# Optimization experiments

Measured on AMD Instinct MI355X. Metric: run time of the kernel, lower is better.

## Reference

```python
import jax, jax.numpy as jnp
import numpy as np

EMBED = 1024
HEADS = 16
HEAD_DIM = EMBED // HEADS


def setup_inputs() -> dict:
    key = jax.random.key(0)
    ks = jax.random.split(key, 12)
    B, S = 2, 2048
    s = 1.0 / np.sqrt(EMBED)
    inp = {
        "query": jax.random.normal(ks[0], (B, S, EMBED), jnp.float32),
        "key_": jax.random.normal(ks[1], (B, S, EMBED), jnp.float32),
        "value": jax.random.normal(ks[2], (B, S, EMBED), jnp.float32),
        "Wq": jax.random.normal(ks[3], (EMBED, EMBED), jnp.float32) * s,
        "bq": jnp.zeros((EMBED,), jnp.float32),
        "Wk": jax.random.normal(ks[4], (EMBED, EMBED), jnp.float32) * s,
        "bk": jnp.zeros((EMBED,), jnp.float32),
        "Wv": jax.random.normal(ks[5], (EMBED, EMBED), jnp.float32) * s,
        "bv": jnp.zeros((EMBED,), jnp.float32),
        "head_mixing": jnp.ones((HEADS, HEADS), jnp.float32) / HEADS,
        "Wo": jax.random.normal(ks[6], (EMBED, EMBED), jnp.float32) * s,
        "bo": jnp.zeros((EMBED,), jnp.float32),
    }
    return inp


def reference(query, key_, value, Wq, bq, Wk, bk, Wv, bv, head_mixing, Wo, bo):
    B, Sq, _ = query.shape
    Sk = key_.shape[1]
    # projections -> [B, H, S, D]
    q = (query @ Wq + bq).reshape(B, Sq, HEADS, HEAD_DIM).transpose(0, 2, 1, 3)
    k = (key_ @ Wk + bk).reshape(B, Sk, HEADS, HEAD_DIM).transpose(0, 2, 1, 3)
    v = (value @ Wv + bv).reshape(B, Sk, HEADS, HEAD_DIM).transpose(0, 2, 1, 3)
    scores = jnp.einsum("bhqd,bhkd->bhqk", q, k) / jnp.sqrt(jnp.float32(HEAD_DIM))
    attn = jax.nn.softmax(scores, axis=-1)  # [B,H,Sq,Sk]; dropout is identity (eval)
    mix = jax.nn.softmax(head_mixing, axis=-1)  # [G,H], softmax over source heads
    mixed = jnp.einsum("bhqk,gh->bgqk", attn, mix)
    ctx = jnp.einsum("bgqk,bgkd->bgqd", mixed, v)  # [B,H,Sq,D]
    ctx = ctx.transpose(0, 2, 1, 3).reshape(B, Sq, EMBED)
    return ctx @ Wo + bo
```

## Files before the change

kernel.cpp:

```cpp
#include <hip/hip_runtime.h>
#include <hip/hip_bf16.h>
#include <cstdint>
#include <cstddef>


typedef __bf16 bf16_t;
typedef __bf16 bf16x8 __attribute__((ext_vector_type(8)));
typedef float f32x4 __attribute__((ext_vector_type(4)));

#define B_ 2
#define S_ 2048
#define E_ 1024
#define H_ 16
#define D_ 64
#define HSTR 18
#define GSTR 580

static __device__ __forceinline__ f32x4 mfma16(bf16x8 a, bf16x8 b, f32x4 c) {
  return __builtin_amdgcn_mfma_f32_16x16x32_bf16(a, b, c, 0, 0, 0);
}

static __device__ __forceinline__ void gload_lds16(const void* g, void* l) {
  __builtin_amdgcn_global_load_lds(
      (const __attribute__((address_space(1))) void*)g,
      (__attribute__((address_space(3))) void*)l, 16, 0, 0);
}

__global__ void mix_kernel(const float* __restrict__ hm, float* __restrict__ mixw) {
  int g = threadIdx.x;
  if (g < H_) {
    float v[H_]; float mx = -1e30f;
    for (int h = 0; h < H_; h++) { v[h] = hm[g * H_ + h]; mx = fmaxf(mx, v[h]); }
    float s = 0.f;
    for (int h = 0; h < H_; h++) { v[h] = __expf(v[h] - mx); s += v[h]; }
    float inv = 1.f / s;
    for (int h = 0; h < H_; h++) mixw[g * H_ + h] = v[h] * inv;
  }
}

__global__ void convw_kernel(const float* __restrict__ w0, const float* __restrict__ w1,
                             const float* __restrict__ w2, const float* __restrict__ w3,
                             bf16_t* __restrict__ t0, bf16_t* __restrict__ t1,
                             bf16_t* __restrict__ t2, bf16_t* __restrict__ t3) {
  __shared__ float t[32][33];
  const int tx = threadIdx.x & 31, ty = threadIdx.x >> 5;
  const int z = blockIdx.z;
  const float* W  = (z == 0) ? w0 : (z == 1) ? w1 : (z == 2) ? w2 : w3;
  bf16_t*      Wt = (z == 0) ? t0 : (z == 1) ? t1 : (z == 2) ? t2 : t3;
  const int k0 = blockIdx.x * 32, n0 = blockIdx.y * 32;
#pragma unroll
  for (int i = 0; i < 4; i++)
    t[ty + i * 8][tx] = W[(size_t)(k0 + ty + i * 8) * E_ + n0 + tx];
  __syncthreads();
#pragma unroll
  for (int i = 0; i < 4; i++)
    Wt[(size_t)(n0 + ty + i * 8) * E_ + k0 + tx] = (bf16_t)t[tx][ty + i * 8];
}

__global__ void convin_kernel(const float* __restrict__ q, const float* __restrict__ k,
                              const float* __restrict__ v,
                              bf16_t* __restrict__ qo, bf16_t* __restrict__ ko,
                              bf16_t* __restrict__ vo) {
  const int z = blockIdx.y;
  const float* src = (z == 0) ? q : (z == 1) ? k : v;
  bf16_t*      dst = (z == 0) ? qo : (z == 1) ? ko : vo;
  const size_t i = ((size_t)blockIdx.x * 256 + threadIdx.x) * 8;
  f32x4 a = *(const f32x4*)&src[i];
  f32x4 b = *(const f32x4*)&src[i + 4];
  bf16x8 o;
#pragma unroll
  for (int j = 0; j < 4; j++) { o[j] = (bf16_t)a[j]; o[4 + j] = (bf16_t)b[j]; }
  *(bf16x8*)&dst[i] = o;
}

__global__ void transpose_v_kernel(const bf16_t* __restrict__ Vp, bf16_t* __restrict__ Vt) {
  __shared__ bf16_t t[32][33];
  const int tx = threadIdx.x & 31, ty = threadIdx.x >> 5;
  const int z = blockIdx.z, b = z >> 4, g = z & 15;
  const int s0 = blockIdx.x * 32, d0 = blockIdx.y * 32;
  const bf16_t* src = Vp + (size_t)b * S_ * E_ + g * 64;
  bf16_t* dst = Vt + (size_t)z * 64 * S_;
#pragma unroll
  for (int i = 0; i < 4; i++)
    t[ty + i * 8][tx] = src[(size_t)(s0 + ty + i * 8) * E_ + d0 + tx];
  __syncthreads();
#pragma unroll
  for (int i = 0; i < 4; i++)
    dst[(size_t)(d0 + ty + i * 8) * S_ + s0 + tx] = t[tx][ty + i * 8];
}

struct GemmSec {
  const void* A; const void* A2; const float* bias; const bf16_t* W; void* C; float scale;
};

template <bool AF32, bool OF32, bool ASUM>
__global__ __launch_bounds__(256) void gemm_kernel(GemmSec s0, GemmSec s1, GemmSec s2) {
  const int z = blockIdx.z;
  GemmSec p = (z == 0) ? s0 : ((z == 1) ? s1 : s2);
  const int tid = threadIdx.x;
  const int wave = tid >> 6, lane = tid & 63;
  const int ln = lane & 15, qd = lane >> 4;
  const int wm = wave >> 1, wn = wave & 1;
  const int row0 = blockIdx.y * 128, col0 = blockIdx.x * 128;

  __shared__ __align__(16) bf16_t As[128 * 32];
  __shared__ __align__(16) bf16_t Bs[128 * 32];

  f32x4 z4 = {0.f, 0.f, 0.f, 0.f};
  f32x4 acc[4][4];
#pragma unroll
  for (int i = 0; i < 4; i++)
#pragma unroll
    for (int j = 0; j < 4; j++) acc[i][j] = z4;

  for (int ks = 0; ks < E_ / 32; ks++) {
    const int kk = ks * 32;
#pragma unroll
    for (int cc = 0; cc < 2; cc++) {
      const int c = tid + cc * 256;
      const int r = c >> 2, kc = (c & 3) * 8;
      if (AF32) {
        const float* Af = (const float*)p.A;
        f32x4 f0 = *(const f32x4*)&Af[(size_t)(row0 + r) * E_ + kk + kc];
        f32x4 f1 = *(const f32x4*)&Af[(size_t)(row0 + r) * E_ + kk + kc + 4];
        if (ASUM) {
          const float* Ag = (const float*)p.A2;
          f0 += *(const f32x4*)&Ag[(size_t)(row0 + r) * E_ + kk + kc];
          f1 += *(const f32x4*)&Ag[(size_t)(row0 + r) * E_ + kk + kc + 4];
        }
        bf16x8 v;
#pragma unroll
        for (int j = 0; j < 4; j++) { v[j] = (bf16_t)f0[j]; v[4 + j] = (bf16_t)f1[j]; }
        *(bf16x8*)&As[r * 32 + kc] = v;
      } else {
        const bf16_t* Ab = (const bf16_t*)p.A;
        gload_lds16(&Ab[(size_t)(row0 + r) * E_ + kk + kc], &As[r * 32 + kc]);
      }
    }
#pragma unroll
    for (int cc = 0; cc < 2; cc++) {
      const int c = tid + cc * 256;
      const int r = c >> 2, kc = (c & 3) * 8;
      gload_lds16(&p.W[(size_t)(col0 + r) * E_ + kk + kc], &Bs[r * 32 + kc]);
    }
    __syncthreads();
    bf16x8 af[4], bfr[4];
#pragma unroll
    for (int mt = 0; mt < 4; mt++) af[mt] = *(const bf16x8*)&As[(wm * 64 + mt * 16 + ln) * 32 + qd * 8];
#pragma unroll
    for (int nt = 0; nt < 4; nt++) bfr[nt] = *(const bf16x8*)&Bs[(wn * 64 + nt * 16 + ln) * 32 + qd * 8];
#pragma unroll
    for (int mt = 0; mt < 4; mt++)
#pragma unroll
      for (int nt = 0; nt < 4; nt++)
        acc[mt][nt] = mfma16(af[mt], bfr[nt], acc[mt][nt]);
    __syncthreads();
  }
#pragma unroll
  for (int nt = 0; nt < 4; nt++) {
    int col = col0 + wn * 64 + nt * 16 + ln;
    float bias_v = p.bias[col];
#pragma unroll
    for (int mt = 0; mt < 4; mt++) {
      int row = row0 + wm * 64 + mt * 16 + qd * 4;
#pragma unroll
      for (int r = 0; r < 4; r++) {
        float v = (acc[mt][nt][r] + bias_v) * p.scale;
        if (OF32) ((float*)p.C)[(size_t)(row + r) * E_ + col] = v;
        else      ((bf16_t*)p.C)[(size_t)(row + r) * E_ + col] = (bf16_t)v;
      }
    }
  }
}

__global__ __launch_bounds__(256, 4) void pass1_kernel(const bf16_t* __restrict__ Qp,
                                                       const bf16_t* __restrict__ Kp,
                                                       float* __restrict__ Z) {
  const int qc = blockIdx.x;
  const int bh = blockIdx.y;
  const int b = bh >> 4, h = bh & 15;
  const int tid = threadIdx.x;
  const int wave = tid >> 6, lane = tid & 63;
  const int ln = lane & 15, qd = lane >> 4;
  const size_t rowbase = (size_t)b * S_;
  const int qbase = qc * 64 + wave * 16;

  bf16x8 qf[2];
#pragma unroll
  for (int db = 0; db < 2; db++)
    qf[db] = *(const bf16x8*)&Qp[(rowbase + qbase + ln) * E_ + h * 64 + db * 32 + qd * 8];

  float l[4] = {0.f, 0.f, 0.f, 0.f};

  for (int kt = 0; kt < S_ / 64; kt++) {
    bf16x8 kf[4][2];
#pragma unroll
    for (int nt = 0; nt < 4; nt++)
#pragma unroll
      for (int db = 0; db < 2; db++)
        kf[nt][db] = *(const bf16x8*)&Kp[(rowbase + kt * 64 + nt * 16 + ln) * E_ + h * 64 + db * 32 + qd * 8];
    f32x4 sc[4];
#pragma unroll
    for (int nt = 0; nt < 4; nt++) {
      f32x4 c0 = {0.f, 0.f, 0.f, 0.f};
      c0 = mfma16(qf[0], kf[nt][0], c0);
      sc[nt] = mfma16(qf[1], kf[nt][1], c0);
    }
#pragma unroll
    for (int r = 0; r < 4; r++)
      l[r] += __expf(sc[0][r]) + __expf(sc[1][r]) + __expf(sc[2][r]) + __expf(sc[3][r]);
  }
#pragma unroll
  for (int r = 0; r < 4; r++) {
    float ll = l[r];
    for (int mask = 1; mask < 16; mask <<= 1) ll += __shfl_xor(ll, mask);
    if (ln == 0) {
      int q = qbase + qd * 4 + r;
      Z[(size_t)bh * S_ + q] = __logf(ll);
    }
  }
}

__global__ __launch_bounds__(512) void pass2_kernel(const bf16_t* __restrict__ Qp,
                                                    const bf16_t* __restrict__ Kp,
                                                    const bf16_t* __restrict__ Vt,
                                                    const float* __restrict__ Z,
                                                    const float* __restrict__ mixw,
                                                    float* __restrict__ pp) {
  const int id = blockIdx.x;
  const int kg = id & 1;
  const int qt = (id >> 1) & 127;
  const int b  = id >> 8;
  const int q0 = qt * 16;

  const int tid = threadIdx.x;
  const int wave = tid >> 6, lane = tid & 63;
  const int ln = lane & 15, qd = lane >> 4;
  const int h0 = wave * 2;

  __shared__ __align__(16) bf16_t Pt[16 * 32 * HSTR];
  __shared__ __align__(16) bf16_t Mx[16 * GSTR];

  const size_t rowbase = (size_t)b * S_;
  const int kbase = kg * (S_ / 2);

  bf16x8 mixA;
#pragma unroll
  for (int j = 0; j < 8; j++) mixA[j] = (bf16_t)0.f;
  if (qd < 2) {
#pragma unroll
    for (int j = 0; j < 8; j++) mixA[j] = (bf16_t)mixw[ln * 16 + qd * 8 + j];
  }

  bf16x8 qf[2][2];
#pragma unroll
  for (int hh = 0; hh < 2; hh++)
#pragma unroll
    for (int db = 0; db < 2; db++)
      qf[hh][db] = *(const bf16x8*)&Qp[(rowbase + q0 + ln) * E_ + (h0 + hh) * 64 + db * 32 + qd * 8];

  float Zr[2][4];
#pragma unroll
  for (int hh = 0; hh < 2; hh++)
#pragma unroll
    for (int r = 0; r < 4; r++)
      Zr[hh][r] = Z[((size_t)(b * H_ + h0 + hh)) * S_ + q0 + qd * 4 + r];

  f32x4 z4 = {0.f, 0.f, 0.f, 0.f};
  f32x4 cacc[2][4];
#pragma unroll
  for (int gg = 0; gg < 2; gg++)
#pragma unroll
    for (int nt = 0; nt < 4; nt++) cacc[gg][nt] = z4;

  const int hsw = (h0 ^ ((qd & 1) << 3));

  for (int t = 0; t < S_ / 64; t++) {
    const int kb = kbase + t * 32;
    uint32_t pk[2][4];
#pragma unroll
    for (int hh = 0; hh < 2; hh++) {
      bf16x8 kf[2][2];
#pragma unroll
      for (int n2 = 0; n2 < 2; n2++)
#pragma unroll
        for (int db = 0; db < 2; db++)
          kf[n2][db] = *(const bf16x8*)&Kp[(rowbase + kb + n2 * 16 + ln) * E_ + (h0 + hh) * 64 + db * 32 + qd * 8];
#pragma unroll
      for (int n2 = 0; n2 < 2; n2++) {
        f32x4 c0;
        c0[0] = -Zr[hh][0]; c0[1] = -Zr[hh][1]; c0[2] = -Zr[hh][2]; c0[3] = -Zr[hh][3];
        c0 = mfma16(qf[hh][0], kf[n2][0], c0);
        c0 = mfma16(qf[hh][1], kf[n2][1], c0);
#pragma unroll
        for (int r = 0; r < 4; r++) {
          uint32_t e = (uint32_t)__builtin_bit_cast(unsigned short, (bf16_t)__expf(c0[r]));
          if (hh == 0) pk[n2][r] = e;
          else         pk[n2][r] |= (e << 16);
        }
      }
    }
#pragma unroll
    for (int n2 = 0; n2 < 2; n2++)
#pragma unroll
      for (int r = 0; r < 4; r++) {
        const int col = (qd * 4 + r) * 32 + n2 * 16 + ln;
        *(uint32_t*)&Pt[col * HSTR + hsw] = pk[n2][r];
      }
    __syncthreads();
    f32x4 mm[4];
#pragma unroll
    for (int i = 0; i < 4; i++) {
      const int cc = wave * 4 + i;
      const int q  = cc >> 1;
      const int k  = (cc & 1) * 16 + ln;
      bf16x8 pb;
      if (qd < 2) {
        const int hblk = (qd * 8) ^ (((q >> 2) & 1) << 3);
        pb = *(const bf16x8*)&Pt[(q * 32 + k) * HSTR + hblk];
      } else {
#pragma unroll
        for (int j = 0; j < 8; j++) pb[j] = (bf16_t)0.f;
      }
      mm[i] = mfma16(mixA, pb, z4);
    }
#pragma unroll
    for (int i = 0; i < 4; i++) {
      const int cc = wave * 4 + i;
      const int q  = cc >> 1;
      const int k  = (cc & 1) * 16 + ln;
#pragma unroll
      for (int r = 0; r < 4; r++)
        Mx[(qd * 4 + r) * GSTR + q * 36 + k] = (bf16_t)mm[i][r];
    }
    __syncthreads();
#pragma unroll
    for (int gg = 0; gg < 2; gg++) {
      bf16x8 af = *(const bf16x8*)&Mx[(h0 + gg) * GSTR + ln * 36 + qd * 8];
#pragma unroll
      for (int nt = 0; nt < 4; nt++) {
        bf16x8 vf = *(const bf16x8*)&Vt[((size_t)((b * H_ + h0 + gg) * 64 + nt * 16 + ln)) * S_ + kb + qd * 8];
        cacc[gg][nt] = mfma16(af, vf, cacc[gg][nt]);
      }
    }
  }
  float* dst = pp + (size_t)kg * B_ * S_ * E_;
#pragma unroll
  for (int gg = 0; gg < 2; gg++)
#pragma unroll
    for (int nt = 0; nt < 4; nt++)
#pragma unroll
      for (int r = 0; r < 4; r++)
        dst[(rowbase + q0 + qd * 4 + r) * E_ + (h0 + gg) * 64 + nt * 16 + ln] = cacc[gg][nt][r];
}

extern "C" void kernel_launch(void* const* d_in, const int* in_sizes, int n_in,
                              void* d_out, int out_size, void* d_ws, size_t ws_size,
                              hipStream_t stream) {
  const float* query = (const float*)d_in[0];
  const float* key_  = (const float*)d_in[1];
  const float* value = (const float*)d_in[2];
  const float* Wq = (const float*)d_in[3];
  const float* bq = (const float*)d_in[4];
  const float* Wk = (const float*)d_in[5];
  const float* bk = (const float*)d_in[6];
  const float* Wv = (const float*)d_in[7];
  const float* bv = (const float*)d_in[8];
  const float* hm = (const float*)d_in[9];
  const float* Wo = (const float*)d_in[10];
  const float* bo = (const float*)d_in[11];
  float* out = (float*)d_out;

  char* ws = (char*)d_ws;
  size_t off = 0;
  auto alloc = [&](size_t bytes) -> void* {
    void* p = ws + off;
    off += (bytes + 255) & ~(size_t)255;
    return p;
  };
  float*  MIXW = (float*) alloc(256 * 4);
  float*  Zb   = (float*) alloc((size_t)B_ * H_ * S_ * 4);
  bf16_t* Qp   = (bf16_t*)alloc((size_t)B_ * S_ * E_ * 2);
  bf16_t* Kp   = (bf16_t*)alloc((size_t)B_ * S_ * E_ * 2);
  bf16_t* Vtt  = (bf16_t*)alloc((size_t)B_ * S_ * E_ * 2);
  bf16_t* Wqt  = (bf16_t*)alloc((size_t)E_ * E_ * 2);
  bf16_t* Wkt  = (bf16_t*)alloc((size_t)E_ * E_ * 2);
  bf16_t* Wvt  = (bf16_t*)alloc((size_t)E_ * E_ * 2);
  bf16_t* Wot  = (bf16_t*)alloc((size_t)E_ * E_ * 2);
  float*  PP   = (float*) alloc((size_t)2 * B_ * S_ * E_ * 4);
  const size_t NELEM = (size_t)B_ * S_ * E_;
  bf16_t* Vp = (bf16_t*)PP;
  bf16_t* Qb = Vp + NELEM;
  bf16_t* Kb = Vp + 2 * NELEM;
  bf16_t* Vb = Vp + 3 * NELEM;
  (void)in_sizes; (void)n_in; (void)out_size; (void)ws_size;

  mix_kernel<<<1, 256, 0, stream>>>(hm, MIXW);
  convw_kernel<<<dim3(32, 32, 4), 256, 0, stream>>>(Wq, Wk, Wv, Wo, Wqt, Wkt, Wvt, Wot);
  convin_kernel<<<dim3(2048, 3), 256, 0, stream>>>(query, key_, value, Qb, Kb, Vb);

  GemmSec sq{Qb, nullptr, bq, Wqt, Qp, 0.125f};
  GemmSec sk{Kb, nullptr, bk, Wkt, Kp, 1.f};
  GemmSec sv{Vb, nullptr, bv, Wvt, Vp, 1.f};
  gemm_kernel<false, false, false><<<dim3(8, 32, 3), 256, 0, stream>>>(sq, sk, sv);

  transpose_v_kernel<<<dim3(64, 2, 32), 256, 0, stream>>>(Vp, Vtt);
  pass1_kernel<<<dim3(32, 32, 1), 256, 0, stream>>>(Qp, Kp, Zb);
  pass2_kernel<<<dim3(512, 1, 1), 512, 0, stream>>>(Qp, Kp, Vtt, Zb, MIXW, PP);

  float* PP1 = PP + (size_t)B_ * S_ * E_;
  GemmSec so{PP, PP1, bo, Wot, out, 1.f};
  gemm_kernel<true, true, true><<<dim3(8, 32, 1), 256, 0, stream>>>(so, so, so);
}
```

Measured before the change: 569.7 us.

## Fuse prep kernels and write transposed V directly from projection GEMM epilogue

Merges the head-mixing softmax, weight transpose/convert and input conversion into one prep kernel, which cuts two launches. It also removes the separate V transpose kernel: the V projection GEMM epilogue writes bf16x4 chunks straight into the per-head transposed layout. This avoids a full read and write of the V projection plus one launch. The trade-off is that the transposed stores are strided across S and may coalesce less well than the original row-major stores.

```diff
diff --git a/kernel.cpp b/kernel.cpp
--- a/kernel.cpp
+++ b/kernel.cpp
@@ -6,6 +6,7 @@
 
 typedef __bf16 bf16_t;
 typedef __bf16 bf16x8 __attribute__((ext_vector_type(8)));
+typedef __bf16 bf16x4 __attribute__((ext_vector_type(4)));
 typedef float f32x4 __attribute__((ext_vector_type(4)));
 
 #define B_ 2
@@ -26,74 +27,64 @@
       (__attribute__((address_space(3))) void*)l, 16, 0, 0);
 }
 
-__global__ void mix_kernel(const float* __restrict__ hm, float* __restrict__ mixw) {
-  int g = threadIdx.x;
-  if (g < H_) {
-    float v[H_]; float mx = -1e30f;
-    for (int h = 0; h < H_; h++) { v[h] = hm[g * H_ + h]; mx = fmaxf(mx, v[h]); }
-    float s = 0.f;
-    for (int h = 0; h < H_; h++) { v[h] = __expf(v[h] - mx); s += v[h]; }
-    float inv = 1.f / s;
-    for (int h = 0; h < H_; h++) mixw[g * H_ + h] = v[h] * inv;
-  }
-}
-
-__global__ void convw_kernel(const float* __restrict__ w0, const float* __restrict__ w1,
-                             const float* __restrict__ w2, const float* __restrict__ w3,
-                             bf16_t* __restrict__ t0, bf16_t* __restrict__ t1,
-                             bf16_t* __restrict__ t2, bf16_t* __restrict__ t3) {
+__global__ void prep_kernel(const float* __restrict__ hm, float* __restrict__ mixw,
+                            const float* __restrict__ w0, const float* __restrict__ w1,
+                            const float* __restrict__ w2, const float* __restrict__ w3,
+                            bf16_t* __restrict__ t0, bf16_t* __restrict__ t1,
+                            bf16_t* __restrict__ t2, bf16_t* __restrict__ t3,
+                            const float* __restrict__ q, const float* __restrict__ k,
+                            const float* __restrict__ v,
+                            bf16_t* __restrict__ qo, bf16_t* __restrict__ ko,
+                            bf16_t* __restrict__ vo) {
   __shared__ float t[32][33];
-  const int tx = threadIdx.x & 31, ty = threadIdx.x >> 5;
+  const int tid = threadIdx.x;
   const int z = blockIdx.z;
-  const float* W  = (z == 0) ? w0 : (z == 1) ? w1 : (z == 2) ? w2 : w3;
-  bf16_t*      Wt = (z == 0) ? t0 : (z == 1) ? t1 : (z == 2) ? t2 : t3;
-  const int k0 = blockIdx.x * 32, n0 = blockIdx.y * 32;
-#pragma unroll
-  for (int i = 0; i < 4; i++)
-    t[ty + i * 8][tx] = W[(size_t)(k0 + ty + i * 8) * E_ + n0 + tx];
-  __syncthreads();
-#pragma unroll
-  for (int i = 0; i < 4; i++)
-    Wt[(size_t)(n0 + ty + i * 8) * E_ + k0 + tx] = (bf16_t)t[tx][ty + i * 8];
-}
-
-__global__ void convin_kernel(const float* __restrict__ q, const float* __restrict__ k,
-                              const float* __restrict__ v,
-                              bf16_t* __restrict__ qo, bf16_t* __restrict__ ko,
-                              bf16_t* __restrict__ vo) {
-  const int z = blockIdx.y;
-  const float* src = (z == 0) ? q : (z == 1) ? k : v;
-  bf16_t*      dst = (z == 0) ? qo : (z == 1) ? ko : vo;
-  const size_t i = ((size_t)blockIdx.x * 256 + threadIdx.x) * 8;
-  f32x4 a = *(const f32x4*)&src[i];
-  f32x4 b = *(const f32x4*)&src[i + 4];
-  bf16x8 o;
-#pragma unroll
-  for (int j = 0; j < 4; j++) { o[j] = (bf16_t)a[j]; o[4 + j] = (bf16_t)b[j]; }
-  *(bf16x8*)&dst[i] = o;
-}
-
-__global__ void transpose_v_kernel(const bf16_t* __restrict__ Vp, bf16_t* __restrict__ Vt) {
-  __shared__ bf16_t t[32][33];
-  const int tx = threadIdx.x & 31, ty = threadIdx.x >> 5;
-  const int z = blockIdx.z, b = z >> 4, g = z & 15;
-  const int s0 = blockIdx.x * 32, d0 = blockIdx.y * 32;
-  const bf16_t* src = Vp + (size_t)b * S_ * E_ + g * 64;
-  bf16_t* dst = Vt + (size_t)z * 64 * S_;
-#pragma unroll
-  for (int i = 0; i < 4; i++)
-    t[ty + i * 8][tx] = src[(size_t)(s0 + ty + i * 8) * E_ + d0 + tx];
-  __syncthreads();
-#pragma unroll
-  for (int i = 0; i < 4; i++)
-    dst[(size_t)(d0 + ty + i * 8) * S_ + s0 + tx] = t[tx][ty + i * 8];
+  if (z < 4) {
+    const int tx = tid & 31, ty = tid >> 5;
+    const float* W  = (z == 0) ? w0 : (z == 1) ? w1 : (z == 2) ? w2 : w3;
+    bf16_t*      Wt = (z == 0) ? t0 : (z == 1) ? t1 : (z == 2) ? t2 : t3;
+    const int k0 = blockIdx.x * 32, n0 = blockIdx.y * 32;
+#pragma unroll
+    for (int i = 0; i < 4; i++)
+      t[ty + i * 8][tx] = W[(size_t)(k0 + ty + i * 8) * E_ + n0 + tx];
+    __syncthreads();
+#pragma unroll
+    for (int i = 0; i < 4; i++)
+      Wt[(size_t)(n0 + ty + i * 8) * E_ + k0 + tx] = (bf16_t)t[tx][ty + i * 8];
+  } else if (z < 7) {
+    const int zz = z - 4;
+    const float* src = (zz == 0) ? q : (zz == 1) ? k : v;
+    bf16_t*      dst = (zz == 0) ? qo : (zz == 1) ? ko : vo;
+    const size_t base = (((size_t)blockIdx.y * 32 + blockIdx.x) * 256 + tid) * 16;
+#pragma unroll
+    for (int c = 0; c < 2; c++) {
+      const size_t i = base + c * 8;
+      f32x4 a = *(const f32x4*)&src[i];
+      f32x4 b = *(const f32x4*)&src[i + 4];
+      bf16x8 o;
+#pragma unroll
+      for (int j = 0; j < 4; j++) { o[j] = (bf16_t)a[j]; o[4 + j] = (bf16_t)b[j]; }
+      *(bf16x8*)&dst[i] = o;
+    }
+  } else if (blockIdx.x == 0 && blockIdx.y == 0) {
+    int g = tid;
+    if (g < H_) {
+      float vv[H_]; float mx = -1e30f;
+      for (int h = 0; h < H_; h++) { vv[h] = hm[g * H_ + h]; mx = fmaxf(mx, vv[h]); }
+      float s = 0.f;
+      for (int h = 0; h < H_; h++) { vv[h] = __expf(vv[h] - mx); s += vv[h]; }
+      float inv = 1.f / s;
+      for (int h = 0; h < H_; h++) mixw[g * H_ + h] = vv[h] * inv;
+    }
+  }
 }
 
 struct GemmSec {
-  const void* A; const void* A2; const float* bias; const bf16_t* W; void* C; float scale;
+  const void* A; const void* A2; const float* bias; const bf16_t* W;
+  void* C; float scale; bf16_t* vt;
 };
 
-template <bool AF32, bool OF32, bool ASUM>
+template <bool AF32, bool OF32, bool ASUM, bool TRV>
 __global__ __launch_bounds__(256) void gemm_kernel(GemmSec s0, GemmSec s1, GemmSec s2) {
   const int z = blockIdx.z;
   GemmSec p = (z == 0) ? s0 : ((z == 1) ? s1 : s2);
@@ -128,19 +119,14 @@
           f0 += *(const f32x4*)&Ag[(size_t)(row0 + r) * E_ + kk + kc];
           f1 += *(const f32x4*)&Ag[(size_t)(row0 + r) * E_ + kk + kc + 4];
         }
-        bf16x8 v;
-#pragma unroll
-        for (int j = 0; j < 4; j++) { v[j] = (bf16_t)f0[j]; v[4 + j] = (bf16_t)f1[j]; }
-        *(bf16x8*)&As[r * 32 + kc] = v;
+        bf16x8 vv;
+#pragma unroll
+        for (int j = 0; j < 4; j++) { vv[j] = (bf16_t)f0[j]; vv[4 + j] = (bf16_t)f1[j]; }
+        *(bf16x8*)&As[r * 32 + kc] = vv;
       } else {
         const bf16_t* Ab = (const bf16_t*)p.A;
         gload_lds16(&Ab[(size_t)(row0 + r) * E_ + kk + kc], &As[r * 32 + kc]);
       }
-    }
-#pragma unroll
-    for (int cc = 0; cc < 2; cc++) {
-      const int c = tid + cc * 256;
-      const int r = c >> 2, kc = (c & 3) * 8;
       gload_lds16(&p.W[(size_t)(col0 + r) * E_ + kk + kc], &Bs[r * 32 + kc]);
     }
     __syncthreads();
@@ -156,18 +142,36 @@
         acc[mt][nt] = mfma16(af[mt], bfr[nt], acc[mt][nt]);
     __syncthreads();
   }
-#pragma unroll
-  for (int nt = 0; nt < 4; nt++) {
-    int col = col0 + wn * 64 + nt * 16 + ln;
-    float bias_v = p.bias[col];
-#pragma unroll
-    for (int mt = 0; mt < 4; mt++) {
-      int row = row0 + wm * 64 + mt * 16 + qd * 4;
-#pragma unroll
-      for (int r = 0; r < 4; r++) {
-        float v = (acc[mt][nt][r] + bias_v) * p.scale;
-        if (OF32) ((float*)p.C)[(size_t)(row + r) * E_ + col] = v;
-        else      ((bf16_t*)p.C)[(size_t)(row + r) * E_ + col] = (bf16_t)v;
+  if (TRV && p.vt) {
+#pragma unroll
+    for (int nt = 0; nt < 4; nt++) {
+      const int col = col0 + wn * 64 + nt * 16 + ln;
+      const int g = col >> 6, d = col & 63;
+      const float bias_v = p.bias[col];
+#pragma unroll
+      for (int mt = 0; mt < 4; mt++) {
+        const int rowb = row0 + wm * 64 + mt * 16 + qd * 4;
+        const int b = rowb >> 11, s = rowb & (S_ - 1);
+        bf16x4 v4;
+#pragma unroll
+        for (int r = 0; r < 4; r++) v4[r] = (bf16_t)((acc[mt][nt][r] + bias_v) * p.scale);
+        *(bf16x4*)&p.vt[((size_t)((b * H_ + g) * 64 + d)) * S_ + s] = v4;
+      }
+    }
+  } else {
+#pragma unroll
+    for (int nt = 0; nt < 4; nt++) {
+      int col = col0 + wn * 64 + nt * 16 + ln;
+      float bias_v = p.bias[col];
+#pragma unroll
+      for (int mt = 0; mt < 4; mt++) {
+        int row = row0 + wm * 64 + mt * 16 + qd * 4;
+#pragma unroll
+        for (int r = 0; r < 4; r++) {
+          float v = (acc[mt][nt][r] + bias_v) * p.scale;
+          if (OF32) ((float*)p.C)[(size_t)(row + r) * E_ + col] = v;
+          else      ((bf16_t*)p.C)[(size_t)(row + r) * E_ + col] = (bf16_t)v;
+        }
       }
     }
   }
@@ -389,26 +393,24 @@
   bf16_t* Wot  = (bf16_t*)alloc((size_t)E_ * E_ * 2);
   float*  PP   = (float*) alloc((size_t)2 * B_ * S_ * E_ * 4);
   const size_t NELEM = (size_t)B_ * S_ * E_;
-  bf16_t* Vp = (bf16_t*)PP;
-  bf16_t* Qb = Vp + NELEM;
-  bf16_t* Kb = Vp + 2 * NELEM;
-  bf16_t* Vb = Vp + 3 * NELEM;
+  bf16_t* Qb = (bf16_t*)PP;
+  bf16_t* Kb = Qb + NELEM;
+  bf16_t* Vb = Qb + 2 * NELEM;
   (void)in_sizes; (void)n_in; (void)out_size; (void)ws_size;
 
-  mix_kernel<<<1, 256, 0, stream>>>(hm, MIXW);
-  convw_kernel<<<dim3(32, 32, 4), 256, 0, stream>>>(Wq, Wk, Wv, Wo, Wqt, Wkt, Wvt, Wot);
-  convin_kernel<<<dim3(2048, 3), 256, 0, stream>>>(query, key_, value, Qb, Kb, Vb);
-
-  GemmSec sq{Qb, nullptr, bq, Wqt, Qp, 0.125f};
-  GemmSec sk{Kb, nullptr, bk, Wkt, Kp, 1.f};
-  GemmSec sv{Vb, nullptr, bv, Wvt, Vp, 1.f};
-  gemm_kernel<false, false, false><<<dim3(8, 32, 3), 256, 0, stream>>>(sq, sk, sv);
-
-  transpose_v_kernel<<<dim3(64, 2, 32), 256, 0, stream>>>(Vp, Vtt);
+  prep_kernel<<<dim3(32, 32, 8), 256, 0, stream>>>(
+      hm, MIXW, Wq, Wk, Wv, Wo, Wqt, Wkt, Wvt, Wot,
+      query, key_, value, Qb, Kb, Vb);
+
+  GemmSec sq{Qb, nullptr, bq, Wqt, Qp, 0.125f, nullptr};
+  GemmSec sk{Kb, nullptr, bk, Wkt, Kp, 1.f, nullptr};
+  GemmSec sv{Vb, nullptr, bv, Wvt, nullptr, 1.f, Vtt};
+  gemm_kernel<false, false, false, true><<<dim3(8, 32, 3), 256, 0, stream>>>(sq, sk, sv);
+
   pass1_kernel<<<dim3(32, 32, 1), 256, 0, stream>>>(Qp, Kp, Zb);
   pass2_kernel<<<dim3(512, 1, 1), 512, 0, stream>>>(Qp, Kp, Vtt, Zb, MIXW, PP);
 
-  float* PP1 = PP + (size_t)B_ * S_ * E_;
-  GemmSec so{PP, PP1, bo, Wot, out, 1.f};
-  gemm_kernel<true, true, true><<<dim3(8, 32, 1), 256, 0, stream>>>(so, so, so);
-}
+  float* PP1 = PP + NELEM;
+  GemmSec so{PP, PP1, bo, Wot, out, 1.f, nullptr};
+  gemm_kernel<true, true, true, false><<<dim3(8, 32, 1), 256, 0, stream>>>(so, so, so);
+}
```

Measured after the change: 579.9 us. About the same (+1.8%).
